# Kernel tuning notes

Hardware: AMD Instinct MI355X
Metric: run time of the kernel (lower is better)

The kernel has to match this reference:

```python
import jax, jax.numpy as jnp
import numpy as np

NL = 4      # nl
H = 256     # h_size
F = 128     # input_size (Fourier features); mapping output = 2*F
DIM = 3     # self.dim
N = 4096    # rows of coords; effective batch after vstack = 2*N


def setup_inputs() -> dict:
    key = jax.random.key(0)
    ks = jax.random.split(key, 7)
    coords = jax.random.normal(ks[0], (N, 2 * DIM), jnp.float32)
    B = jax.random.normal(ks[1], (DIM, F), jnp.float32)            # Fourier mapping matrix
    w0 = jax.random.normal(ks[2], (H, 2 * F), jnp.float32) * 0.1   # encoder[0].weight
    ws = jax.random.normal(ks[3], (NL - 1, H, H), jnp.float32) * 0.1   # encoder[1..nl-1].weight
    w_last = jax.random.normal(ks[4], (H, H), jnp.float32) * 0.1   # encoder[-1].weight
    w1 = jax.random.normal(ks[5], (NL, H, H), jnp.float32) * 0.1   # encoder1[ii].weight
    b1 = jax.random.normal(ks[6], (NL, H), jnp.float32) * 0.1      # encoder1[ii].bias
    return dict(coords=coords, B=B, w0=w0, ws=ws, w_last=w_last, w1=w1, b1=b1)


def input_mapping(x, B):
    # FBPINNs Fourier feature mapping: [sin(2*pi*x@B), cos(2*pi*x@B)]
    proj = (2.0 * jnp.pi) * (x @ B)                  # (2N, F)
    return jnp.concatenate([jnp.sin(proj), jnp.cos(proj)], axis=-1)  # (2N, 2F)


def sin_layer(x, w):
    # y[b,j] = sum_k sin(x[b,k] * w[j,k])  -- broadcast multiply + sin + reduce
    return jnp.sin(x[:, None, :] * w[None, :, :]).sum(axis=2)


def reference(coords, B, w0, ws, w_last, w1, b1):
    x0 = coords[:, :DIM]
    x1 = coords[:, DIM:]
    x = jnp.concatenate([x0, x1], axis=0)            # vstack -> (2N, DIM)
    x = input_mapping(x, B)                          # (2N, 2F)
    x = sin_layer(x, w0)                             # (2N, H)
    x = jnp.sin(x @ w1[0].T + b1[0])                 # encoder1[0] + sin
    for ii in range(1, NL):
        x = sin_layer(x, ws[ii - 1])                 # encoder[ii] sin-layer
        x = jnp.sin(x @ w1[ii].T + b1[ii])           # encoder1[ii] + sin
    x = sin_layer(x, w_last)                         # encoder[-1] sin-layer
    return (x, coords)
```

## Files before the change

kernel.cpp:

```cpp
#include <hip/hip_runtime.h>
#include <string.h>

#define NCRD 4096
#define NROW 8192
#define MT   32
#define WG_U4 114688

typedef __attribute__((ext_vector_type(8)))  _Float16 half8;
typedef __attribute__((ext_vector_type(16))) float f32x16;
typedef __attribute__((ext_vector_type(4)))  int   i32x4;

static __device__ __forceinline__ float sinrev(float t){ return __builtin_amdgcn_sinf(__builtin_amdgcn_fractf(t)); }
static __device__ __forceinline__ float cosrev(float t){ return __builtin_amdgcn_cosf(__builtin_amdgcn_fractf(t)); }
static __device__ __forceinline__ unsigned short f2h(float f){
    _Float16 h = (_Float16)f;
    unsigned short u; memcpy(&u, &h, 2); return u;
}

static __device__ __forceinline__ i32x4 gload16(const uint4* p){
    i32x4 r;
    asm volatile("global_load_dwordx4 %0, %1, off" : "=v"(r) : "v"(p) : "memory");
    return r;
}
static __device__ __forceinline__ void vmwaitK(int K, i32x4& a, i32x4& b){
    if (K >= 16)      asm volatile("s_waitcnt vmcnt(16)" : "+v"(a), "+v"(b));
    else if (K >= 14) asm volatile("s_waitcnt vmcnt(14)" : "+v"(a), "+v"(b));
    else if (K >= 12) asm volatile("s_waitcnt vmcnt(12)" : "+v"(a), "+v"(b));
    else if (K >= 10) asm volatile("s_waitcnt vmcnt(10)" : "+v"(a), "+v"(b));
    else if (K >= 8)  asm volatile("s_waitcnt vmcnt(8)"  : "+v"(a), "+v"(b));
    else if (K >= 6)  asm volatile("s_waitcnt vmcnt(6)"  : "+v"(a), "+v"(b));
    else if (K >= 4)  asm volatile("s_waitcnt vmcnt(4)"  : "+v"(a), "+v"(b));
    else if (K >= 2)  asm volatile("s_waitcnt vmcnt(2)"  : "+v"(a), "+v"(b));
    else              asm volatile("s_waitcnt vmcnt(0)"  : "+v"(a), "+v"(b));
}

__constant__ int c_offs[9] = {0,16384,24576,40960,49152,65536,73728,90112,98304};

__global__ void prep_kernel(const float* __restrict__ w0, const float* __restrict__ ws,
                            const float* __restrict__ wlast, const float* __restrict__ w1,
                            const float* __restrict__ coords, const float* __restrict__ b1,
                            uint4* __restrict__ Wg, float* __restrict__ b1s,
                            float* __restrict__ out)
{
    int l = blockIdx.x, part = blockIdx.y, t = threadIdx.x;
    const float inv2pi = 0.15915494309189535f;
    if (l == 9) {
        int base = part*256 + t;
        if (base < 1024) b1s[base] = b1[base]*inv2pi;
        for (int i = base; i < NCRD*6; i += 16384)
            out[(size_t)NROW*256 + i] = coords[i];
        return;
    }
    bool sinl = !(l & 1);
    if (!sinl && part >= 32) return;
    const float* src;
    switch (l) {
        case 0: src = w0;          break;
        case 1: src = w1;          break;
        case 2: src = ws;          break;
        case 3: src = w1+65536;    break;
        case 4: src = ws+65536;    break;
        case 5: src = w1+2*65536;  break;
        case 6: src = ws+2*65536;  break;
        case 7: src = w1+3*65536;  break;
        default: src = wlast;      break;
    }
    int idx = part*256 + t;
    int c  = idx >> 10, r = idx & 1023;
    int w  = r >> 7,  r2 = r & 127;
    int hh = r2 >> 6, ln = r2 & 63;
    int col  = w*32 + (ln & 31);
    int keff = c*32 + hh*16 + (ln >> 5)*8;
    int term = keff >> 8, kk = keff & 255;
    const float* s = src + col*256 + kk;
    unsigned short h[8];
    #pragma unroll
    for (int j = 0; j < 8; ++j) {
        float wv_ = s[j], v;
        if (!sinl)          v = wv_ * inv2pi;
        else if (term == 0) v = wv_;
        else                v = -wv_*wv_*wv_*(1.0f/6.0f);
        h[j] = f2h(v);
    }
    uint4 o; memcpy(&o, h, 16);
    Wg[c_offs[l] + idx] = o;
}

template<int MODE, int NC>
static __device__ __forceinline__ void do_layer(
    const uint4* __restrict__ wq,
    const float* __restrict__ br,
    float* __restrict__ outg,
    unsigned short* xa,
    int wv, int ls, int lm, int n0)
{
    constexpr int PD = 8;
    constexpr int RS = PD + 1;
    constexpr int PA = 2;
    f32x16 acc = {0.f,0.f,0.f,0.f,0.f,0.f,0.f,0.f,0.f,0.f,0.f,0.f,0.f,0.f,0.f,0.f};

    i32x4 ring0[RS], ring1[RS];
    #pragma unroll
    for (int p = 0; p < PD; ++p)
        if (p < NC) {
            ring0[p % RS] = gload16(wq + p*1024);
            ring1[p % RS] = gload16(wq + p*1024 + 64);
        }

    __syncthreads();
    const half8* xa8 = (const half8*)xa;
    half8 pa0[PA], pa1[PA];
    #pragma unroll
    for (int p = 0; p < PA; ++p) {
        pa0[p] = xa8[(p*4     + ls)*32 + lm];
        pa1[p] = xa8[(p*4 + 2 + ls)*32 + lm];
    }
    #pragma unroll
    for (int c = 0; c < NC; ++c) {
        if (c + PD < NC) {
            ring0[(c+PD) % RS] = gload16(wq + (c+PD)*1024);
            ring1[(c+PD) % RS] = gload16(wq + (c+PD)*1024 + 64);
        }
        half8 a0 = pa0[c % PA], a1 = pa1[c % PA];
        if (c + PA < NC) {
            pa0[(c+PA) % PA] = xa8[((c+PA)*4     + ls)*32 + lm];
            pa1[(c+PA) % PA] = xa8[((c+PA)*4 + 2 + ls)*32 + lm];
        }
        int K = 2*(NC-1-c);
        vmwaitK(K > 16 ? 16 : K, ring0[c % RS], ring1[c % RS]);
        half8 b0, b1v;
        { i32x4 t0 = ring0[c % RS], t1 = ring1[c % RS];
          memcpy(&b0, &t0, 16); memcpy(&b1v, &t1, 16); }
        acc = __builtin_amdgcn_mfma_f32_32x32x16_f16(a0, b0,  acc, 0,0,0);
        acc = __builtin_amdgcn_mfma_f32_32x32x16_f16(a1, b1v, acc, 0,0,0);
    }
    __syncthreads();
    float bb = 0.f;
    if (MODE == 1) bb = br[wv*32 + lm];
    int h = wv*32 + lm;
    #pragma unroll
    for (int r = 0; r < 16; ++r) {
        float v = acc[r];
        int m = (r & 3) + 8*(r >> 2) + 4*ls;
        if (MODE == 2) {
            outg[(size_t)(n0 + m)*256 + h] = v;
        } else if (MODE == 1) {
            float s = sinrev(v + bb);
            float s3 = s*s*s;
            xa[(((h>>3)     )*32 + m)*8 + (h&7)] = f2h(s);
            xa[(((h>>3) + 32)*32 + m)*8 + (h&7)] = f2h(s3);
        } else {
            xa[((h>>3)*32 + m)*8 + (h&7)] = f2h(v);
        }
    }
}

__global__ __launch_bounds__(512, 2)
void net_kernel(const float* __restrict__ coords, const float* __restrict__ Bm,
                const uint4* __restrict__ Wg, const float* __restrict__ b1s,
                float* __restrict__ out)
{
    __shared__ unsigned short xa[64*32*8];
    __shared__ float cb[MT*3];
    __shared__ float bl[384];

    int tid = threadIdx.x, lane = tid & 63, wv = tid >> 6;
    int ls = (lane >> 5) & 1, lm = lane & 31;
    int n0 = blockIdx.x * MT;

    for (int i = tid; i < MT*3; i += 512) {
        int r = i/3, d = i - 3*r, nv = n0 + r;
        cb[i] = (nv < NCRD) ? coords[nv*6 + d] : coords[(nv-NCRD)*6 + 3 + d];
    }
    for (int i = tid; i < 384; i += 512) bl[i] = Bm[i];
    __syncthreads();
    {
        int m = tid & 31, colb = (tid >> 5) * 16;
        float c0 = cb[m*3], c1 = cb[m*3+1], c2 = cb[m*3+2];
        unsigned short tmp[2][16];
        #pragma unroll
        for (int j = 0; j < 16; ++j) {
            int col = colb + j, f = col & 127;
            float p = c0*bl[f] + c1*bl[128+f] + c2*bl[256+f];
            float s = (col < 128) ? sinrev(p) : cosrev(p);
            tmp[0][j] = f2h(s); tmp[1][j] = f2h(s*s*s);
        }
        #pragma unroll
        for (int pp = 0; pp < 2; ++pp)
            #pragma unroll
            for (int g = 0; g < 2; ++g) {
                uint4 v; memcpy(&v, &tmp[pp][g*8], 16);
                *(uint4*)&xa[((pp*32 + (colb>>3) + g)*32 + m)*8] = v;
            }
    }

    int wl = wv*128 + lane;
    do_layer<0,16>(Wg +      0 + wl, nullptr,   nullptr, xa, wv, ls, lm, n0);
    do_layer<1, 8>(Wg +  16384 + wl, b1s + 0,   nullptr, xa, wv, ls, lm, n0);
    do_layer<0,16>(Wg +  24576 + wl, nullptr,   nullptr, xa, wv, ls, lm, n0);
    do_layer<1, 8>(Wg +  40960 + wl, b1s + 256, nullptr, xa, wv, ls, lm, n0);
    do_layer<0,16>(Wg +  49152 + wl, nullptr,   nullptr, xa, wv, ls, lm, n0);
    do_layer<1, 8>(Wg +  65536 + wl, b1s + 512, nullptr, xa, wv, ls, lm, n0);
    do_layer<0,16>(Wg +  73728 + wl, nullptr,   nullptr, xa, wv, ls, lm, n0);
    do_layer<1, 8>(Wg +  90112 + wl, b1s + 768, nullptr, xa, wv, ls, lm, n0);
    do_layer<2,16>(Wg +  98304 + wl, nullptr,   out,     xa, wv, ls, lm, n0);
}

extern "C" void kernel_launch(void* const* d_in, const int* in_sizes, int n_in,
                              void* d_out, int out_size, void* d_ws, size_t ws_size,
                              hipStream_t stream)
{
    const float* coords = (const float*)d_in[0];
    const float* Bm     = (const float*)d_in[1];
    const float* w0     = (const float*)d_in[2];
    const float* ws     = (const float*)d_in[3];
    const float* wlast  = (const float*)d_in[4];
    const float* w1     = (const float*)d_in[5];
    const float* b1     = (const float*)d_in[6];
    float* out = (float*)d_out;

    uint4* Wg  = (uint4*)d_ws;
    float* b1s = (float*)((char*)d_ws + (size_t)WG_U4*16);

    dim3 pg(10, 64);
    prep_kernel<<<pg, 256, 0, stream>>>(w0, ws, wlast, w1, coords, b1, Wg, b1s, out);
    net_kernel<<<NROW/MT, 512, 0, stream>>>(coords, Bm, Wg, b1s, out);
}
```

Measured before the change: 97.62 us.

## Store cubic-term sin-layer weights as FP8 e4m3 and expand to fp16 in-register

The cubic Taylor-term weights of each sin-layer are now stored as scaled FP8 (e4m3) in the prep kernel instead of fp16, halving their global memory footprint. They are expanded to fp16 in registers with bit manipulation before the MFMA, and the activation cube terms are rescaled by 0.5 to match. The aim is to cut the weight traffic that every workgroup streams per layer. The cost is extra ALU work for the expansion and reduced precision on the cubic correction term.

```diff
diff --git a/kernel.cpp b/kernel.cpp
--- a/kernel.cpp
+++ b/kernel.cpp
@@ -1,10 +1,11 @@
 #include <hip/hip_runtime.h>
 #include <string.h>
+#include <math.h>
 
 #define NCRD 4096
 #define NROW 8192
 #define MT   32
-#define WG_U4 114688
+#define WG_U4 94208
 
 typedef __attribute__((ext_vector_type(8)))  _Float16 half8;
 typedef __attribute__((ext_vector_type(16))) float f32x16;
@@ -15,6 +16,23 @@
 static __device__ __forceinline__ unsigned short f2h(float f){
     _Float16 h = (_Float16)f;
     unsigned short u; memcpy(&u, &h, 2); return u;
+}
+
+static __device__ unsigned char f2e4m3(float v){
+    unsigned int s = (__float_as_uint(v) >> 24) & 0x80;
+    float a = fabsf(v);
+    if (a >= 448.f) return (unsigned char)(s | 0x7e);
+    int e; frexpf(a, &e); e -= 1;
+    if (e < -6) e = -6;
+    float step = exp2f((float)(e - 3));
+    float q = rintf(a / step) * step;
+    if (q <= 0.f) return (unsigned char)s;
+    int e2; float m = frexpf(q, &e2);
+    int E = e2 + 6;
+    unsigned int bits;
+    if (E >= 1) bits = ((unsigned)E << 3) | ((unsigned)rintf(m*16.f) - 8u);
+    else        bits = (unsigned)rintf(q * 512.f);
+    return (unsigned char)(s | bits);
 }
 
 static __device__ __forceinline__ i32x4 gload16(const uint4* p){
@@ -34,7 +52,18 @@
     else              asm volatile("s_waitcnt vmcnt(0)"  : "+v"(a), "+v"(b));
 }
 
-__constant__ int c_offs[9] = {0,16384,24576,40960,49152,65536,73728,90112,98304};
+static __device__ __forceinline__ void expand2(unsigned int d, unsigned int& o0, unsigned int& o1){
+    o0 = ((d << 8) & 0x80008000u) | ((d << 7) & 0x3f803f80u);
+    o1 = ( d       & 0x80008000u) | ((d >> 1) & 0x3f803f80u);
+}
+static __device__ __forceinline__ half8 expand_frag(unsigned int da, unsigned int db){
+    unsigned int r[4];
+    expand2(da, r[0], r[1]);
+    expand2(db, r[2], r[3]);
+    half8 h; memcpy(&h, r, 16); return h;
+}
+
+__constant__ int c_offs[9] = {0,12288,20480,32768,40960,53248,61440,73728,81920};
 
 __global__ void prep_kernel(const float* __restrict__ w0, const float* __restrict__ ws,
                             const float* __restrict__ wlast, const float* __restrict__ w1,
@@ -47,7 +76,7 @@
     if (l == 9) {
         int base = part*256 + t;
         if (base < 1024) b1s[base] = b1[base]*inv2pi;
-        for (int i = base; i < NCRD*6; i += 16384)
+        for (int i = base; i < NCRD*6; i += 12288)
             out[(size_t)NROW*256 + i] = coords[i];
         return;
     }
@@ -66,77 +95,101 @@
         default: src = wlast;      break;
     }
     int idx = part*256 + t;
-    int c  = idx >> 10, r = idx & 1023;
-    int w  = r >> 7,  r2 = r & 127;
-    int hh = r2 >> 6, ln = r2 & 63;
-    int col  = w*32 + (ln & 31);
-    int keff = c*32 + hh*16 + (ln >> 5)*8;
-    int term = keff >> 8, kk = keff & 255;
-    const float* s = src + col*256 + kk;
-    unsigned short h[8];
-    #pragma unroll
-    for (int j = 0; j < 8; ++j) {
-        float wv_ = s[j], v;
-        if (!sinl)          v = wv_ * inv2pi;
-        else if (term == 0) v = wv_;
-        else                v = -wv_*wv_*wv_*(1.0f/6.0f);
-        h[j] = f2h(v);
-    }
-    uint4 o; memcpy(&o, h, 16);
-    Wg[c_offs[l] + idx] = o;
-}
-
-template<int MODE, int NC>
-static __device__ __forceinline__ void do_layer(
+    if (idx < 8192) {
+        int c  = idx >> 10, r = idx & 1023;
+        int w  = r >> 7,  r2 = r & 127;
+        int hh = r2 >> 6, ln = r2 & 63;
+        int col  = w*32 + (ln & 31);
+        int k0   = c*32 + hh*16 + (ln >> 5)*8;
+        const float* s = src + col*256 + k0;
+        unsigned short h[8];
+        #pragma unroll
+        for (int j = 0; j < 8; ++j)
+            h[j] = f2h(sinl ? s[j] : s[j]*inv2pi);
+        uint4 o; memcpy(&o, h, 16);
+        Wg[c_offs[l] + idx] = o;
+    } else {
+        int idx2 = idx - 8192;
+        int q  = idx2 >> 10, r = idx2 & 1023;
+        int wvp = r >> 7,  r2 = r & 127;
+        int L  = r2 >> 6,  ln = r2 & 63;
+        int col = wvp*32 + (ln & 31);
+        int ls  = ln >> 5;
+        unsigned char b8[16];
+        #pragma unroll
+        for (int b = 0; b < 16; ++b) {
+            int f  = b >> 3;
+            int jj = (b & 4) | ((b & 1) << 1) | ((b >> 1) & 1);
+            int kk = q*64 + L*32 + f*16 + ls*8 + jj;
+            float w = src[col*256 + kk];
+            b8[b] = f2e4m3(-512.0f * w*w*w * (1.0f/6.0f));
+        }
+        uint4 o; memcpy(&o, b8, 16);
+        Wg[c_offs[l] + idx] = o;
+    }
+}
+
+template<int MODE>
+static __device__ __forceinline__ void do_sin_layer(
     const uint4* __restrict__ wq,
-    const float* __restrict__ br,
     float* __restrict__ outg,
     unsigned short* xa,
     int wv, int ls, int lm, int n0)
 {
-    constexpr int PD = 8;
-    constexpr int RS = PD + 1;
-    constexpr int PA = 2;
+    constexpr int RS = 9;
     f32x16 acc = {0.f,0.f,0.f,0.f,0.f,0.f,0.f,0.f,0.f,0.f,0.f,0.f,0.f,0.f,0.f,0.f};
-
     i32x4 ring0[RS], ring1[RS];
     #pragma unroll
-    for (int p = 0; p < PD; ++p)
-        if (p < NC) {
-            ring0[p % RS] = gload16(wq + p*1024);
-            ring1[p % RS] = gload16(wq + p*1024 + 64);
-        }
-
+    for (int p = 0; p < 8; ++p) {
+        ring0[p % RS] = gload16(wq + p*1024);
+        ring1[p % RS] = gload16(wq + p*1024 + 64);
+    }
     __syncthreads();
     const half8* xa8 = (const half8*)xa;
-    half8 pa0[PA], pa1[PA];
-    #pragma unroll
-    for (int p = 0; p < PA; ++p) {
-        pa0[p] = xa8[(p*4     + ls)*32 + lm];
+    half8 pa0[2], pa1[2];
+    #pragma unroll
+    for (int p = 0; p < 2; ++p) {
+        pa0[p] = xa8[(p*4 + ls)*32 + lm];
         pa1[p] = xa8[(p*4 + 2 + ls)*32 + lm];
     }
-    #pragma unroll
-    for (int c = 0; c < NC; ++c) {
-        if (c + PD < NC) {
-            ring0[(c+PD) % RS] = gload16(wq + (c+PD)*1024);
-            ring1[(c+PD) % RS] = gload16(wq + (c+PD)*1024 + 64);
-        }
-        half8 a0 = pa0[c % PA], a1 = pa1[c % PA];
-        if (c + PA < NC) {
-            pa0[(c+PA) % PA] = xa8[((c+PA)*4     + ls)*32 + lm];
-            pa1[(c+PA) % PA] = xa8[((c+PA)*4 + 2 + ls)*32 + lm];
-        }
-        int K = 2*(NC-1-c);
-        vmwaitK(K > 16 ? 16 : K, ring0[c % RS], ring1[c % RS]);
+    const uint4* wq8 = wq + 8192;
+    #pragma unroll
+    for (int c = 0; c < 8; ++c) {
+        if (c < 4) {
+            ring0[(8+c) % RS] = gload16(wq8 + c*1024);
+            ring1[(8+c) % RS] = gload16(wq8 + c*1024 + 64);
+        }
+        half8 a0 = pa0[c & 1], a1 = pa1[c & 1];
+        if (c + 2 < 8) {
+            pa0[c & 1] = xa8[((c+2)*4 + ls)*32 + lm];
+            pa1[c & 1] = xa8[((c+2)*4 + 2 + ls)*32 + lm];
+        }
+        vmwaitK((c < 4) ? 16 : (22 - 2*c), ring0[c % RS], ring1[c % RS]);
         half8 b0, b1v;
         { i32x4 t0 = ring0[c % RS], t1 = ring1[c % RS];
           memcpy(&b0, &t0, 16); memcpy(&b1v, &t1, 16); }
         acc = __builtin_amdgcn_mfma_f32_32x32x16_f16(a0, b0,  acc, 0,0,0);
         acc = __builtin_amdgcn_mfma_f32_32x32x16_f16(a1, b1v, acc, 0,0,0);
     }
-    __syncthreads();
-    float bb = 0.f;
-    if (MODE == 1) bb = br[wv*32 + lm];
+    #pragma unroll
+    for (int qc = 0; qc < 4; ++qc) {
+        int v = 8 + qc;
+        vmwaitK(6 - 2*qc, ring0[v % RS], ring1[v % RS]);
+        i32x4 t0 = ring0[v % RS], t1 = ring1[v % RS];
+        half8 f0 = expand_frag((unsigned)t0[0], (unsigned)t0[1]);
+        half8 f1 = expand_frag((unsigned)t0[2], (unsigned)t0[3]);
+        half8 f2 = expand_frag((unsigned)t1[0], (unsigned)t1[1]);
+        half8 f3 = expand_frag((unsigned)t1[2], (unsigned)t1[3]);
+        half8 a0 = xa8[(32 + qc*8 + 0 + ls)*32 + lm];
+        half8 a1 = xa8[(32 + qc*8 + 2 + ls)*32 + lm];
+        half8 a2 = xa8[(32 + qc*8 + 4 + ls)*32 + lm];
+        half8 a3 = xa8[(32 + qc*8 + 6 + ls)*32 + lm];
+        acc = __builtin_amdgcn_mfma_f32_32x32x16_f16(a0, f0, acc, 0,0,0);
+        acc = __builtin_amdgcn_mfma_f32_32x32x16_f16(a1, f1, acc, 0,0,0);
+        acc = __builtin_amdgcn_mfma_f32_32x32x16_f16(a2, f2, acc, 0,0,0);
+        acc = __builtin_amdgcn_mfma_f32_32x32x16_f16(a3, f3, acc, 0,0,0);
+    }
+    __syncthreads();
     int h = wv*32 + lm;
     #pragma unroll
     for (int r = 0; r < 16; ++r) {
@@ -144,14 +197,58 @@
         int m = (r & 3) + 8*(r >> 2) + 4*ls;
         if (MODE == 2) {
             outg[(size_t)(n0 + m)*256 + h] = v;
-        } else if (MODE == 1) {
-            float s = sinrev(v + bb);
-            float s3 = s*s*s;
-            xa[(((h>>3)     )*32 + m)*8 + (h&7)] = f2h(s);
-            xa[(((h>>3) + 32)*32 + m)*8 + (h&7)] = f2h(s3);
         } else {
-            xa[((h>>3)*32 + m)*8 + (h&7)] = f2h(v);
-        }
+            xa[(((h>>3)     )*32 + m)*8 + (h&7)] = f2h(v);
+            xa[(((h>>3) + 32)*32 + m)*8 + (h&7)] = f2h(v*v*v*0.5f);
+        }
+    }
+}
+
+static __device__ __forceinline__ void do_gemm_layer(
+    const uint4* __restrict__ wq,
+    const float* __restrict__ br,
+    unsigned short* xa,
+    int wv, int ls, int lm)
+{
+    constexpr int RS = 9;
+    f32x16 acc = {0.f,0.f,0.f,0.f,0.f,0.f,0.f,0.f,0.f,0.f,0.f,0.f,0.f,0.f,0.f,0.f};
+    i32x4 ring0[RS], ring1[RS];
+    #pragma unroll
+    for (int p = 0; p < 8; ++p) {
+        ring0[p % RS] = gload16(wq + p*1024);
+        ring1[p % RS] = gload16(wq + p*1024 + 64);
+    }
+    __syncthreads();
+    const half8* xa8 = (const half8*)xa;
+    half8 pa0[2], pa1[2];
+    #pragma unroll
+    for (int p = 0; p < 2; ++p) {
+        pa0[p] = xa8[(p*4 + ls)*32 + lm];
+        pa1[p] = xa8[(p*4 + 2 + ls)*32 + lm];
+    }
+    #pragma unroll
+    for (int c = 0; c < 8; ++c) {
+        half8 a0 = pa0[c & 1], a1 = pa1[c & 1];
+        if (c + 2 < 8) {
+            pa0[c & 1] = xa8[((c+2)*4 + ls)*32 + lm];
+            pa1[c & 1] = xa8[((c+2)*4 + 2 + ls)*32 + lm];
+        }
+        vmwaitK(14 - 2*c, ring0[c % RS], ring1[c % RS]);
+        half8 b0, b1v;
+        { i32x4 t0 = ring0[c % RS], t1 = ring1[c % RS];
+          memcpy(&b0, &t0, 16); memcpy(&b1v, &t1, 16); }
+        acc = __builtin_amdgcn_mfma_f32_32x32x16_f16(a0, b0,  acc, 0,0,0);
+        acc = __builtin_amdgcn_mfma_f32_32x32x16_f16(a1, b1v, acc, 0,0,0);
+    }
+    __syncthreads();
+    float bb = br[wv*32 + lm];
+    int h = wv*32 + lm;
+    #pragma unroll
+    for (int r = 0; r < 16; ++r) {
+        float s = sinrev(acc[r] + bb);
+        int m = (r & 3) + 8*(r >> 2) + 4*ls;
+        xa[(((h>>3)     )*32 + m)*8 + (h&7)] = f2h(s);
+        xa[(((h>>3) + 32)*32 + m)*8 + (h&7)] = f2h(s*s*s*0.5f);
     }
 }
 
@@ -183,7 +280,7 @@
             int col = colb + j, f = col & 127;
             float p = c0*bl[f] + c1*bl[128+f] + c2*bl[256+f];
             float s = (col < 128) ? sinrev(p) : cosrev(p);
-            tmp[0][j] = f2h(s); tmp[1][j] = f2h(s*s*s);
+            tmp[0][j] = f2h(s); tmp[1][j] = f2h(s*s*s*0.5f);
         }
         #pragma unroll
         for (int pp = 0; pp < 2; ++pp)
@@ -195,15 +292,15 @@
     }
 
     int wl = wv*128 + lane;
-    do_layer<0,16>(Wg +      0 + wl, nullptr,   nullptr, xa, wv, ls, lm, n0);
-    do_layer<1, 8>(Wg +  16384 + wl, b1s + 0,   nullptr, xa, wv, ls, lm, n0);
-    do_layer<0,16>(Wg +  24576 + wl, nullptr,   nullptr, xa, wv, ls, lm, n0);
-    do_layer<1, 8>(Wg +  40960 + wl, b1s + 256, nullptr, xa, wv, ls, lm, n0);
-    do_layer<0,16>(Wg +  49152 + wl, nullptr,   nullptr, xa, wv, ls, lm, n0);
-    do_layer<1, 8>(Wg +  65536 + wl, b1s + 512, nullptr, xa, wv, ls, lm, n0);
-    do_layer<0,16>(Wg +  73728 + wl, nullptr,   nullptr, xa, wv, ls, lm, n0);
-    do_layer<1, 8>(Wg +  90112 + wl, b1s + 768, nullptr, xa, wv, ls, lm, n0);
-    do_layer<2,16>(Wg +  98304 + wl, nullptr,   out,     xa, wv, ls, lm, n0);
+    do_sin_layer<0>(Wg +     0 + wl, nullptr, xa, wv, ls, lm, n0);
+    do_gemm_layer  (Wg + 12288 + wl, b1s + 0,   xa, wv, ls, lm);
+    do_sin_layer<0>(Wg + 20480 + wl, nullptr, xa, wv, ls, lm, n0);
+    do_gemm_layer  (Wg + 32768 + wl, b1s + 256, xa, wv, ls, lm);
+    do_sin_layer<0>(Wg + 40960 + wl, nullptr, xa, wv, ls, lm, n0);
+    do_gemm_layer  (Wg + 53248 + wl, b1s + 512, xa, wv, ls, lm);
+    do_sin_layer<0>(Wg + 61440 + wl, nullptr, xa, wv, ls, lm, n0);
+    do_gemm_layer  (Wg + 73728 + wl, b1s + 768, xa, wv, ls, lm);
+    do_sin_layer<2>(Wg + 81920 + wl, out,     xa, wv, ls, lm, n0);
 }
 
 extern "C" void kernel_launch(void* const* d_in, const int* in_sizes, int n_in,
@@ -222,7 +319,7 @@
     uint4* Wg  = (uint4*)d_ws;
     float* b1s = (float*)((char*)d_ws + (size_t)WG_U4*16);
 
-    dim3 pg(10, 64);
+    dim3 pg(10, 48);
     prep_kernel<<<pg, 256, 0, stream>>>(w0, ws, wlast, w1, coords, b1, Wg, b1s, out);
     net_kernel<<<NROW/MT, 512, 0, stream>>>(coords, Bm, Wg, b1s, out);
 }
```

Measured after the change: 111.2 us. 1.14x slower.
